# Optimization experiments

Hardware: AMD Instinct MI355X
Metric: run time of the kernel (lower is better)

## Reference

```python
import jax, jax.numpy as jnp
import numpy as np
import math

B, Q, CQ = 2, 2048, 512
H, D = 8, 64  # no_heads, c_hidden

def setup_inputs() -> dict:
    key = jax.random.key(0)
    ks = jax.random.split(key, 8)
    s = 0.02
    return {
        "q_x": jax.random.normal(ks[0], (B, Q, CQ), jnp.float32),
        "kv_x": jax.random.normal(ks[1], (B, Q, CQ), jnp.float32),
        "bias": jax.random.normal(ks[2], (B, 1, Q, Q), jnp.float32),
        "w_qkv": jax.random.normal(ks[3], (3 * H * D, CQ), jnp.float32) * s,
        "w_o": jax.random.normal(ks[4], (CQ, H * D), jnp.float32) * s,
        "b_o": jnp.zeros((CQ,), jnp.float32),
        "w_g": jax.random.normal(ks[5], (H * D, CQ), jnp.float32) * s,
        "b_g": jnp.zeros((H * D,), jnp.float32),
    }

def reference(q_x, kv_x, bias, w_qkv, w_o, b_o, w_g, b_g):
    # Fused QKV projection from q_x (kv_x is unused by the original module's _prep_qkv)
    qkv = jnp.einsum('bqc,ec->bqe', q_x, w_qkv)  # [B,Q,3*H*D]
    q, k, v = jnp.split(qkv, 3, axis=-1)
    q = q.reshape(B, Q, H, D) / math.sqrt(D)
    k = k.reshape(B, Q, H, D)
    v = v.reshape(B, Q, H, D)
    # scores + additive pairwise bias, softmax over keys
    scores = jnp.einsum('bqhd,bkhd->bhqk', q, k) + bias  # [B,H,Q,K]
    attn = jax.nn.softmax(scores, axis=-1)
    o = jnp.einsum('bhqk,bkhd->bqhd', attn, v)  # [B,Q,H,D]
    # sigmoid gating
    g = jax.nn.sigmoid(jnp.einsum('bqc,ec->bqe', q_x, w_g) + b_g).reshape(B, Q, H, D)
    o = o * g
    # output projection
    o = o.reshape(B, Q, H * D)
    return jnp.einsum('bqe,ce->bqc', o, w_o) + b_o
```

## Files before the change

kernel.cpp:

```cpp
#include <hip/hip_runtime.h>
#include <math.h>

#define B_  2
#define Q_  2048
#define CQ_ 512
#define H_  8
#define D_  64
#define M_  (B_*Q_)
#define L2E 1.44269504088896f

typedef __bf16 bf16;
typedef __bf16 bf16x4 __attribute__((ext_vector_type(4)));
typedef __bf16 bf16x8 __attribute__((ext_vector_type(8)));
typedef float  f32x4  __attribute__((ext_vector_type(4)));

__device__ __forceinline__ void gl_lds16(const bf16* g, bf16* l) {
    __builtin_amdgcn_global_load_lds(
        (const __attribute__((address_space(1))) unsigned int*)g,
        (__attribute__((address_space(3))) unsigned int*)l, 16, 0, 0);
}

#define S0 (4096*512)
#define S1 (1536*512)
#define S2 (512*512)
#define S3 (512*512)
__global__ __launch_bounds__(256)
void convert_kernel(const float* __restrict__ qx, const float* __restrict__ wqkv,
                    const float* __restrict__ wg, const float* __restrict__ wo,
                    bf16* __restrict__ qxb, bf16* __restrict__ wcat, bf16* __restrict__ wob)
{
    const long long t = (long long)blockIdx.x * 256 + threadIdx.x;
    const long long e = t * 8;
    const float* src; bf16* dst;
    if (e < S0)                { src = qx + e;                  dst = qxb + e; }
    else if (e < S0 + S1)      { src = wqkv + (e - S0);         dst = wcat + (e - S0); }
    else if (e < S0 + S1 + S2) { src = wg + (e - S0 - S1);      dst = wcat + S1 + (e - S0 - S1); }
    else                       { src = wo + (e - S0 - S1 - S2); dst = wob + (e - S0 - S1 - S2); }
    const float4 a = *(const float4*)(src);
    const float4 b = *(const float4*)(src + 4);
    bf16x8 v;
    v[0] = (bf16)a.x; v[1] = (bf16)a.y; v[2] = (bf16)a.z; v[3] = (bf16)a.w;
    v[4] = (bf16)b.x; v[5] = (bf16)b.y; v[6] = (bf16)b.z; v[7] = (bf16)b.w;
    *(bf16x8*)dst = v;
}

template<int BM, int BN, int EPI>
__global__ __launch_bounds__(256)
void gemm_bf16(const bf16* __restrict__ A, const bf16* __restrict__ W,
               const float* __restrict__ bvec, float* __restrict__ fout,
               bf16* __restrict__ qb, bf16* __restrict__ kb, bf16* __restrict__ vb,
               bf16* __restrict__ gb)
{
    constexpr int MI = BM / 32, NJ = BN / 32;
    __shared__ __align__(16) bf16 As[BM * 32];
    __shared__ __align__(16) bf16 Bs[BN * 32];

    const int t = threadIdx.x;
    const int w = t >> 6, lane = t & 63;
    const int l15 = lane & 15, quad = lane >> 4;
    const int wm = w & 1, wn = w >> 1;
    const int bm = blockIdx.x * BM;
    const int bn = blockIdx.y * BN;

    f32x4 acc[MI][NJ] = {};

    const int rr = t >> 2;
    const int cc = (t & 3) * 8;

    for (int k0 = 0; k0 < 512; k0 += 32) {
        #pragma unroll
        for (int i = 0; i < BM / 64; ++i)
            gl_lds16(A + (size_t)(bm + i * 64 + rr) * 512 + k0 + cc,
                     As + (i * 64 + w * 16) * 32);
        #pragma unroll
        for (int i = 0; i < BN / 64; ++i)
            gl_lds16(W + (size_t)(bn + i * 64 + rr) * 512 + k0 + cc,
                     Bs + (i * 64 + w * 16) * 32);
        __asm__ volatile("s_waitcnt vmcnt(0)" ::: "memory");
        __syncthreads();

        bf16x8 af[MI], bfr[NJ];
        #pragma unroll
        for (int i = 0; i < MI; ++i)
            af[i] = *(const bf16x8*)(As + (wm * (BM / 2) + i * 16 + l15) * 32 + quad * 8);
        #pragma unroll
        for (int j = 0; j < NJ; ++j)
            bfr[j] = *(const bf16x8*)(Bs + (wn * (BN / 2) + j * 16 + l15) * 32 + quad * 8);
        #pragma unroll
        for (int i = 0; i < MI; ++i)
            #pragma unroll
            for (int j = 0; j < NJ; ++j)
                acc[i][j] = __builtin_amdgcn_mfma_f32_16x16x32_bf16(af[i], bfr[j], acc[i][j], 0, 0, 0);
        __syncthreads();
    }

    #pragma unroll
    for (int i = 0; i < MI; ++i) {
        #pragma unroll
        for (int r = 0; r < 4; ++r) {
            const int m = bm + wm * (BM / 2) + i * 16 + quad * 4 + r;
            const int b = m >> 11, qq = m & 2047;
            #pragma unroll
            for (int j = 0; j < NJ; ++j) {
                const int n = bn + wn * (BN / 2) + j * 16 + l15;
                const float cval = acc[i][j][r];
                if constexpr (EPI == 0) {
                    const int part = n >> 9;
                    const int h = (n >> 6) & 7, d = n & 63;
                    const size_t bhbase = (size_t)(b * H_ + h) * (Q_ * D_);
                    if (part == 0) {
                        qb[bhbase + (size_t)qq * D_ + d] = (bf16)(cval * (0.125f * L2E));
                    } else if (part == 1) {
                        const int rg = qq >> 4, ll = qq & 15, ch = d >> 3, jj = d & 7;
                        kb[bhbase + rg * 1024 + ch * 128 + ll * 8 + jj] = (bf16)cval;
                    } else if (part == 2) {
                        const int tile = qq >> 6, kc2 = (qq & 63) >> 3, jj = qq & 7;
                        const int dt = d >> 4, dl = d & 15;
                        vb[bhbase + tile * 4096 + dt * 1024 + kc2 * 128 + dl * 8 + jj] = (bf16)cval;
                    } else {
                        const int gcol = n & 511;
                        const float x = cval + bvec[gcol];
                        gb[(size_t)m * 512 + gcol] = (bf16)(1.f / (1.f + __expf(-x)));
                    }
                } else {
                    fout[(size_t)m * 512 + n] = cval + bvec[n];
                }
            }
        }
    }
}

__global__ __launch_bounds__(256, 2)
void attn_kernel(const bf16* __restrict__ qb, const bf16* __restrict__ kf,
                 const bf16* __restrict__ vf, const float* __restrict__ bias,
                 const bf16* __restrict__ g, bf16* __restrict__ og)
{
    __shared__ __align__(16) bf16 Ps[4][16 * 72];

    const int tid  = threadIdx.x;
    const int wv   = tid >> 6, lane = tid & 63;
    const int l15  = lane & 15, quad = lane >> 4;
    const int x    = blockIdx.x;
    const int bh   = ((x & 1) << 3) | (x >> 1);
    const int b    = bh >> 3, h = bh & 7;
    const int qrow = blockIdx.y * 64 + wv * 16 + l15;

    const bf16* qptr = qb + ((size_t)bh * Q_ + qrow) * D_;
    const bf16x8 bq0 = *(const bf16x8*)(qptr + quad * 8);
    const bf16x8 bq1 = *(const bf16x8*)(qptr + 32 + quad * 8);

    f32x4 acc[4] = {};
    float m_run = -INFINITY, l_run = 0.f;

    const bf16*  kfb  = kf + (size_t)bh * (Q_ * D_);
    const bf16*  vfb  = vf + (size_t)bh * (Q_ * D_);
    const float* brow = bias + ((size_t)b * Q_ + qrow) * Q_;

    bf16x8 kc[8], vc[8], kn[8], vn[8];
    float4 bc[4], bn4[4];

    #pragma unroll
    for (int kt = 0; kt < 4; ++kt) {
        kc[kt * 2]     = *(const bf16x8*)(kfb + (kt * 8 + quad) * 128 + l15 * 8);
        kc[kt * 2 + 1] = *(const bf16x8*)(kfb + (kt * 8 + quad + 4) * 128 + l15 * 8);
        vc[kt * 2]     = *(const bf16x8*)(vfb + (kt * 8 + quad) * 128 + l15 * 8);
        vc[kt * 2 + 1] = *(const bf16x8*)(vfb + (kt * 8 + quad + 4) * 128 + l15 * 8);
        bc[kt] = *(const float4*)(brow + kt * 16 + quad * 4);
    }

    bf16* pw = Ps[wv] + l15 * 72;

    #pragma unroll 2
    for (int t = 0; t < 32; ++t) {
        if (t < 31) {
            const int off = (t + 1) * 4096;
            const int boff = (t + 1) * 64;
            #pragma unroll
            for (int kt = 0; kt < 4; ++kt) {
                kn[kt * 2]     = *(const bf16x8*)(kfb + off + (kt * 8 + quad) * 128 + l15 * 8);
                kn[kt * 2 + 1] = *(const bf16x8*)(kfb + off + (kt * 8 + quad + 4) * 128 + l15 * 8);
                vn[kt * 2]     = *(const bf16x8*)(vfb + off + (kt * 8 + quad) * 128 + l15 * 8);
                vn[kt * 2 + 1] = *(const bf16x8*)(vfb + off + (kt * 8 + quad + 4) * 128 + l15 * 8);
                bn4[kt] = *(const float4*)(brow + boff + kt * 16 + quad * 4);
            }
        }

        float sc[4][4];
        #pragma unroll
        for (int kt = 0; kt < 4; ++kt) {
            f32x4 sacc = {0.f, 0.f, 0.f, 0.f};
            sacc = __builtin_amdgcn_mfma_f32_16x16x32_bf16(kc[kt * 2],     bq0, sacc, 0, 0, 0);
            sacc = __builtin_amdgcn_mfma_f32_16x16x32_bf16(kc[kt * 2 + 1], bq1, sacc, 0, 0, 0);
            sc[kt][0] = fmaf(bc[kt].x, L2E, sacc[0]);
            sc[kt][1] = fmaf(bc[kt].y, L2E, sacc[1]);
            sc[kt][2] = fmaf(bc[kt].z, L2E, sacc[2]);
            sc[kt][3] = fmaf(bc[kt].w, L2E, sacc[3]);
        }

        float tmax = -INFINITY;
        #pragma unroll
        for (int kt = 0; kt < 4; ++kt)
            tmax = fmaxf(tmax, fmaxf(fmaxf(sc[kt][0], sc[kt][1]),
                                     fmaxf(sc[kt][2], sc[kt][3])));
        tmax = fmaxf(tmax, __shfl_xor(tmax, 16, 64));
        tmax = fmaxf(tmax, __shfl_xor(tmax, 32, 64));

        const float mn = fmaxf(m_run, tmax);
        const float alpha = __builtin_amdgcn_exp2f(m_run - mn);
        m_run = mn;

        float rsum = 0.f;
        #pragma unroll
        for (int kt = 0; kt < 4; ++kt)
            #pragma unroll
            for (int r = 0; r < 4; ++r) {
                sc[kt][r] = __builtin_amdgcn_exp2f(sc[kt][r] - mn);
                rsum += sc[kt][r];
            }
        rsum += __shfl_xor(rsum, 16, 64);
        rsum += __shfl_xor(rsum, 32, 64);
        l_run = l_run * alpha + rsum;
        #pragma unroll
        for (int dt = 0; dt < 4; ++dt) acc[dt] *= alpha;

        #pragma unroll
        for (int kt = 0; kt < 4; ++kt) {
            bf16x4 p4;
            p4[0] = (bf16)sc[kt][0]; p4[1] = (bf16)sc[kt][1];
            p4[2] = (bf16)sc[kt][2]; p4[3] = (bf16)sc[kt][3];
            *(bf16x4*)(pw + kt * 16 + quad * 4) = p4;
        }
        __asm__ volatile("s_waitcnt lgkmcnt(0)" ::: "memory");

        #pragma unroll
        for (int kt2 = 0; kt2 < 2; ++kt2) {
            const bf16x8 bp = *(const bf16x8*)(pw + kt2 * 32 + quad * 8);
            #pragma unroll
            for (int dt = 0; dt < 4; ++dt)
                acc[dt] = __builtin_amdgcn_mfma_f32_16x16x32_bf16(vc[dt * 2 + kt2], bp, acc[dt], 0, 0, 0);
        }

        if (t < 31) {
            #pragma unroll
            for (int i = 0; i < 8; ++i) { kc[i] = kn[i]; vc[i] = vn[i]; }
            #pragma unroll
            for (int kt = 0; kt < 4; ++kt) bc[kt] = bn4[kt];
        }
    }

    const float inv = 1.f / l_run;
    const size_t obase = ((size_t)(b * Q_ + qrow)) * 512 + h * 64;
    #pragma unroll
    for (int dt = 0; dt < 4; ++dt) {
        const bf16x4 gv = *(const bf16x4*)(g + obase + dt * 16 + quad * 4);
        bf16x4 ov;
        #pragma unroll
        for (int r = 0; r < 4; ++r)
            ov[r] = (bf16)(acc[dt][r] * inv * (float)gv[r]);
        *(bf16x4*)(og + obase + dt * 16 + quad * 4) = ov;
    }
}

extern "C" void kernel_launch(void* const* d_in, const int* in_sizes, int n_in,
                              void* d_out, int out_size, void* d_ws, size_t ws_size,
                              hipStream_t stream)
{
    const float* q_x   = (const float*)d_in[0];
    const float* bias  = (const float*)d_in[2];
    const float* w_qkv = (const float*)d_in[3];
    const float* w_o   = (const float*)d_in[4];
    const float* b_o   = (const float*)d_in[5];
    const float* w_g   = (const float*)d_in[6];
    const float* b_g   = (const float*)d_in[7];
    float* out = (float*)d_out;

    char* ws = (char*)d_ws;
    bf16* qxb  = (bf16*)(ws);
    bf16* wcat = (bf16*)(ws + (4u  << 20));
    bf16* wob  = (bf16*)(ws + (6u  << 20));
    bf16* qb   = (bf16*)(ws + (8u  << 20));
    bf16* kb   = (bf16*)(ws + (12u << 20));
    bf16* vb   = (bf16*)(ws + (16u << 20));
    bf16* gb   = (bf16*)(ws + (20u << 20));
    bf16* ogb  = (bf16*)(ws + (24u << 20));

    convert_kernel<<<(S0 + S1 + S2 + S3) / (256 * 8), 256, 0, stream>>>(
        q_x, w_qkv, w_g, w_o, qxb, wcat, wob);
    gemm_bf16<128, 128, 0><<<dim3(32, 16), 256, 0, stream>>>(
        qxb, wcat, b_g, nullptr, qb, kb, vb, gb);
    attn_kernel<<<dim3(B_ * H_, Q_ / 64), 256, 0, stream>>>(qb, kb, vb, bias, gb, ogb);
    gemm_bf16<64, 128, 1><<<dim3(64, 4), 256, 0, stream>>>(
        ogb, wob, b_o, out, nullptr, nullptr, nullptr, nullptr);
}
```

Before: 205.3 us.

## Stage K/V tiles in LDS with 32x32 MFMA and 128-row query blocks

The attention kernel now loads each 64-key K/V tile once per block into double-buffered LDS through global_load_lds, and all four waves share it. Before, every wave pulled K/V straight from global into registers. Each wave now handles 32 query rows using 32x32x16 MFMAs, and the grid is halved to 128 query rows per block. The QKV GEMM epilogue writes K and V in a new swizzled layout that matches the new MFMA operand order. The cost is a block-wide barrier every iteration, occupancy dropped to one block per SIMD group in launch bounds, and fewer blocks (256), which may underfill the GPU.

```diff
diff --git a/kernel.cpp b/kernel.cpp
--- a/kernel.cpp
+++ b/kernel.cpp
@@ -13,6 +13,7 @@
 typedef __bf16 bf16x4 __attribute__((ext_vector_type(4)));
 typedef __bf16 bf16x8 __attribute__((ext_vector_type(8)));
 typedef float  f32x4  __attribute__((ext_vector_type(4)));
+typedef float  f32x16 __attribute__((ext_vector_type(16)));
 
 __device__ __forceinline__ void gl_lds16(const bf16* g, bf16* l) {
     __builtin_amdgcn_global_load_lds(
@@ -111,12 +112,13 @@
                     if (part == 0) {
                         qb[bhbase + (size_t)qq * D_ + d] = (bf16)(cval * (0.125f * L2E));
                     } else if (part == 1) {
-                        const int rg = qq >> 4, ll = qq & 15, ch = d >> 3, jj = d & 7;
-                        kb[bhbase + rg * 1024 + ch * 128 + ll * 8 + jj] = (bf16)cval;
+                        kb[bhbase + (qq >> 6) * 4096 + ((qq >> 5) & 1) * 2048
+                           + (d >> 4) * 512 + ((d >> 3) & 1) * 256
+                           + (qq & 31) * 8 + (d & 7)] = (bf16)cval;
                     } else if (part == 2) {
-                        const int tile = qq >> 6, kc2 = (qq & 63) >> 3, jj = qq & 7;
-                        const int dt = d >> 4, dl = d & 15;
-                        vb[bhbase + tile * 4096 + dt * 1024 + kc2 * 128 + dl * 8 + jj] = (bf16)cval;
+                        vb[bhbase + (qq >> 6) * 4096 + (d >> 5) * 2048
+                           + ((qq & 63) >> 4) * 512 + ((qq >> 3) & 1) * 256
+                           + (d & 31) * 8 + (qq & 7)] = (bf16)cval;
                     } else {
                         const int gcol = n & 511;
                         const float x = cval + bvec[gcol];
@@ -130,79 +132,92 @@
     }
 }
 
-__global__ __launch_bounds__(256, 2)
+__global__ __launch_bounds__(256, 1)
 void attn_kernel(const bf16* __restrict__ qb, const bf16* __restrict__ kf,
                  const bf16* __restrict__ vf, const float* __restrict__ bias,
                  const bf16* __restrict__ g, bf16* __restrict__ og)
 {
-    __shared__ __align__(16) bf16 Ps[4][16 * 72];
+    __shared__ __align__(16) bf16 Ks[2][4096];
+    __shared__ __align__(16) bf16 Vs[2][4096];
+    __shared__ __align__(16) bf16 Ps[4][32 * 72];
 
     const int tid  = threadIdx.x;
     const int wv   = tid >> 6, lane = tid & 63;
-    const int l15  = lane & 15, quad = lane >> 4;
+    const int l31  = lane & 31, b5 = lane >> 5;
     const int x    = blockIdx.x;
-    const int bh   = ((x & 1) << 3) | (x >> 1);
+    const int bh   = ((x & 7) << 1) | (x >> 3);
     const int b    = bh >> 3, h = bh & 7;
-    const int qrow = blockIdx.y * 64 + wv * 16 + l15;
-
-    const bf16* qptr = qb + ((size_t)bh * Q_ + qrow) * D_;
-    const bf16x8 bq0 = *(const bf16x8*)(qptr + quad * 8);
-    const bf16x8 bq1 = *(const bf16x8*)(qptr + 32 + quad * 8);
-
-    f32x4 acc[4] = {};
+    const int qg   = blockIdx.y * 128 + wv * 32 + l31;
+
+    const bf16* qp = qb + ((size_t)bh * Q_ + qg) * D_;
+    bf16x8 bq[4];
+    #pragma unroll
+    for (int c = 0; c < 4; ++c)
+        bq[c] = *(const bf16x8*)(qp + c * 16 + b5 * 8);
+
+    f32x16 acc[2] = {};
     float m_run = -INFINITY, l_run = 0.f;
 
     const bf16*  kfb  = kf + (size_t)bh * (Q_ * D_);
     const bf16*  vfb  = vf + (size_t)bh * (Q_ * D_);
-    const float* brow = bias + ((size_t)b * Q_ + qrow) * Q_;
-
-    bf16x8 kc[8], vc[8], kn[8], vn[8];
-    float4 bc[4], bn4[4];
-
-    #pragma unroll
-    for (int kt = 0; kt < 4; ++kt) {
-        kc[kt * 2]     = *(const bf16x8*)(kfb + (kt * 8 + quad) * 128 + l15 * 8);
-        kc[kt * 2 + 1] = *(const bf16x8*)(kfb + (kt * 8 + quad + 4) * 128 + l15 * 8);
-        vc[kt * 2]     = *(const bf16x8*)(vfb + (kt * 8 + quad) * 128 + l15 * 8);
-        vc[kt * 2 + 1] = *(const bf16x8*)(vfb + (kt * 8 + quad + 4) * 128 + l15 * 8);
-        bc[kt] = *(const float4*)(brow + kt * 16 + quad * 4);
+    const float* brow = bias + ((size_t)b * Q_ + qg) * Q_;
+
+    f32x4 bcur[8], bnxt[8];
+
+    #pragma unroll
+    for (int p = 0; p < 2; ++p) {
+        gl_lds16(kfb + (wv * 2 + p) * 512 + lane * 8, Ks[0] + (wv * 2 + p) * 512);
+        gl_lds16(vfb + (wv * 2 + p) * 512 + lane * 8, Vs[0] + (wv * 2 + p) * 512);
     }
-
-    bf16* pw = Ps[wv] + l15 * 72;
-
-    #pragma unroll 2
+    #pragma unroll
+    for (int i = 0; i < 8; ++i)
+        bcur[i] = *(const f32x4*)(brow + (i >> 2) * 32 + (i & 3) * 8 + b5 * 4);
+    __asm__ volatile("s_waitcnt vmcnt(0)" ::: "memory");
+    __syncthreads();
+
+    bf16* pw = Ps[wv] + l31 * 72;
+
+    int cur = 0;
+    #pragma unroll 1
     for (int t = 0; t < 32; ++t) {
         if (t < 31) {
-            const int off = (t + 1) * 4096;
-            const int boff = (t + 1) * 64;
-            #pragma unroll
-            for (int kt = 0; kt < 4; ++kt) {
-                kn[kt * 2]     = *(const bf16x8*)(kfb + off + (kt * 8 + quad) * 128 + l15 * 8);
-                kn[kt * 2 + 1] = *(const bf16x8*)(kfb + off + (kt * 8 + quad + 4) * 128 + l15 * 8);
-                vn[kt * 2]     = *(const bf16x8*)(vfb + off + (kt * 8 + quad) * 128 + l15 * 8);
-                vn[kt * 2 + 1] = *(const bf16x8*)(vfb + off + (kt * 8 + quad + 4) * 128 + l15 * 8);
-                bn4[kt] = *(const float4*)(brow + boff + kt * 16 + quad * 4);
-            }
-        }
-
-        float sc[4][4];
-        #pragma unroll
-        for (int kt = 0; kt < 4; ++kt) {
-            f32x4 sacc = {0.f, 0.f, 0.f, 0.f};
-            sacc = __builtin_amdgcn_mfma_f32_16x16x32_bf16(kc[kt * 2],     bq0, sacc, 0, 0, 0);
-            sacc = __builtin_amdgcn_mfma_f32_16x16x32_bf16(kc[kt * 2 + 1], bq1, sacc, 0, 0, 0);
-            sc[kt][0] = fmaf(bc[kt].x, L2E, sacc[0]);
-            sc[kt][1] = fmaf(bc[kt].y, L2E, sacc[1]);
-            sc[kt][2] = fmaf(bc[kt].z, L2E, sacc[2]);
-            sc[kt][3] = fmaf(bc[kt].w, L2E, sacc[3]);
-        }
+            const size_t off = (size_t)(t + 1) * 4096;
+            #pragma unroll
+            for (int p = 0; p < 2; ++p) {
+                gl_lds16(kfb + off + (wv * 2 + p) * 512 + lane * 8,
+                         Ks[cur ^ 1] + (wv * 2 + p) * 512);
+                gl_lds16(vfb + off + (wv * 2 + p) * 512 + lane * 8,
+                         Vs[cur ^ 1] + (wv * 2 + p) * 512);
+            }
+            const int k0n = (t + 1) * 64;
+            #pragma unroll
+            for (int i = 0; i < 8; ++i)
+                bnxt[i] = *(const f32x4*)(brow + k0n + (i >> 2) * 32 + (i & 3) * 8 + b5 * 4);
+        }
+
+        const bf16* Kc = Ks[cur];
+        f32x16 sv[2] = {};
+        #pragma unroll
+        for (int kg = 0; kg < 2; ++kg)
+            #pragma unroll
+            for (int c = 0; c < 4; ++c) {
+                const bf16x8 ak = *(const bf16x8*)(Kc + kg * 2048 + c * 512 + lane * 8);
+                sv[kg] = __builtin_amdgcn_mfma_f32_32x32x16_bf16(ak, bq[c], sv[kg], 0, 0, 0);
+            }
+
+        float sc[2][16];
+        #pragma unroll
+        for (int kg = 0; kg < 2; ++kg)
+            #pragma unroll
+            for (int r = 0; r < 16; ++r)
+                sc[kg][r] = fmaf(bcur[kg * 4 + (r >> 2)][r & 3], L2E, sv[kg][r]);
 
         float tmax = -INFINITY;
         #pragma unroll
-        for (int kt = 0; kt < 4; ++kt)
-            tmax = fmaxf(tmax, fmaxf(fmaxf(sc[kt][0], sc[kt][1]),
-                                     fmaxf(sc[kt][2], sc[kt][3])));
-        tmax = fmaxf(tmax, __shfl_xor(tmax, 16, 64));
+        for (int kg = 0; kg < 2; ++kg)
+            #pragma unroll
+            for (int r = 0; r < 16; ++r)
+                tmax = fmaxf(tmax, sc[kg][r]);
         tmax = fmaxf(tmax, __shfl_xor(tmax, 32, 64));
 
         const float mn = fmaxf(m_run, tmax);
@@ -211,54 +226,64 @@
 
         float rsum = 0.f;
         #pragma unroll
-        for (int kt = 0; kt < 4; ++kt)
-            #pragma unroll
-            for (int r = 0; r < 4; ++r) {
-                sc[kt][r] = __builtin_amdgcn_exp2f(sc[kt][r] - mn);
-                rsum += sc[kt][r];
-            }
-        rsum += __shfl_xor(rsum, 16, 64);
+        for (int kg = 0; kg < 2; ++kg)
+            #pragma unroll
+            for (int r = 0; r < 16; ++r) {
+                sc[kg][r] = __builtin_amdgcn_exp2f(sc[kg][r] - mn);
+                rsum += sc[kg][r];
+            }
         rsum += __shfl_xor(rsum, 32, 64);
         l_run = l_run * alpha + rsum;
-        #pragma unroll
-        for (int dt = 0; dt < 4; ++dt) acc[dt] *= alpha;
-
-        #pragma unroll
-        for (int kt = 0; kt < 4; ++kt) {
-            bf16x4 p4;
-            p4[0] = (bf16)sc[kt][0]; p4[1] = (bf16)sc[kt][1];
-            p4[2] = (bf16)sc[kt][2]; p4[3] = (bf16)sc[kt][3];
-            *(bf16x4*)(pw + kt * 16 + quad * 4) = p4;
-        }
+        acc[0] *= alpha;
+        acc[1] *= alpha;
+
+        #pragma unroll
+        for (int kg = 0; kg < 2; ++kg)
+            #pragma unroll
+            for (int gi = 0; gi < 4; ++gi) {
+                bf16x4 p4;
+                p4[0] = (bf16)sc[kg][gi * 4 + 0];
+                p4[1] = (bf16)sc[kg][gi * 4 + 1];
+                p4[2] = (bf16)sc[kg][gi * 4 + 2];
+                p4[3] = (bf16)sc[kg][gi * 4 + 3];
+                *(bf16x4*)(pw + kg * 32 + gi * 8 + b5 * 4) = p4;
+            }
         __asm__ volatile("s_waitcnt lgkmcnt(0)" ::: "memory");
 
-        #pragma unroll
-        for (int kt2 = 0; kt2 < 2; ++kt2) {
-            const bf16x8 bp = *(const bf16x8*)(pw + kt2 * 32 + quad * 8);
-            #pragma unroll
-            for (int dt = 0; dt < 4; ++dt)
-                acc[dt] = __builtin_amdgcn_mfma_f32_16x16x32_bf16(vc[dt * 2 + kt2], bp, acc[dt], 0, 0, 0);
+        const bf16* Vc = Vs[cur];
+        #pragma unroll
+        for (int c4 = 0; c4 < 4; ++c4) {
+            const bf16x8 bp = *(const bf16x8*)(pw + c4 * 16 + b5 * 8);
+            #pragma unroll
+            for (int dg = 0; dg < 2; ++dg) {
+                const bf16x8 av = *(const bf16x8*)(Vc + dg * 2048 + c4 * 512 + lane * 8);
+                acc[dg] = __builtin_amdgcn_mfma_f32_32x32x16_bf16(av, bp, acc[dg], 0, 0, 0);
+            }
         }
 
         if (t < 31) {
             #pragma unroll
-            for (int i = 0; i < 8; ++i) { kc[i] = kn[i]; vc[i] = vn[i]; }
-            #pragma unroll
-            for (int kt = 0; kt < 4; ++kt) bc[kt] = bn4[kt];
-        }
+            for (int i = 0; i < 8; ++i) bcur[i] = bnxt[i];
+        }
+        __asm__ volatile("s_waitcnt vmcnt(0)" ::: "memory");
+        __syncthreads();
+        cur ^= 1;
     }
 
     const float inv = 1.f / l_run;
-    const size_t obase = ((size_t)(b * Q_ + qrow)) * 512 + h * 64;
-    #pragma unroll
-    for (int dt = 0; dt < 4; ++dt) {
-        const bf16x4 gv = *(const bf16x4*)(g + obase + dt * 16 + quad * 4);
-        bf16x4 ov;
-        #pragma unroll
-        for (int r = 0; r < 4; ++r)
-            ov[r] = (bf16)(acc[dt][r] * inv * (float)gv[r]);
-        *(bf16x4*)(og + obase + dt * 16 + quad * 4) = ov;
-    }
+    const size_t obase = ((size_t)(b * Q_ + qg)) * 512 + h * 64;
+    #pragma unroll
+    for (int dg = 0; dg < 2; ++dg)
+        #pragma unroll
+        for (int gi = 0; gi < 4; ++gi) {
+            const int d0 = dg * 32 + gi * 8 + b5 * 4;
+            const bf16x4 gv = *(const bf16x4*)(g + obase + d0);
+            bf16x4 ov;
+            #pragma unroll
+            for (int r = 0; r < 4; ++r)
+                ov[r] = (bf16)(acc[dg][gi * 4 + r] * inv * (float)gv[r]);
+            *(bf16x4*)(og + obase + d0) = ov;
+        }
 }
 
 extern "C" void kernel_launch(void* const* d_in, const int* in_sizes, int n_in,
@@ -288,7 +313,7 @@
         q_x, w_qkv, w_g, w_o, qxb, wcat, wob);
     gemm_bf16<128, 128, 0><<<dim3(32, 16), 256, 0, stream>>>(
         qxb, wcat, b_g, nullptr, qb, kb, vb, gb);
-    attn_kernel<<<dim3(B_ * H_, Q_ / 64), 256, 0, stream>>>(qb, kb, vb, bias, gb, ogb);
+    attn_kernel<<<dim3(B_ * H_, Q_ / 128), 256, 0, stream>>>(qb, kb, vb, bias, gb, ogb);
     gemm_bf16<64, 128, 1><<<dim3(64, 4), 256, 0, stream>>>(
         ogb, wob, b_o, out, nullptr, nullptr, nullptr, nullptr);
 }
```

New measurement: 214.6 us. 1.05x slower.
